# Performance work log

Hardware: AMD Instinct MI355X
Metric: run time of the kernel (lower is better)

Reference implementation:

```python
import jax, jax.numpy as jnp
import numpy as np
from jax import lax

F32 = jnp.float32
N_BATCH = 131072

# spiking gate algebra on {0,1} floats (matches VecAND/VecOR/VecXOR/VecNOT/VecMUX)
def OR(a, b):
    return a + b - a * b

def XOR(a, b):
    return a + b - 2.0 * a * b

def or_all(x):
    # OR-tree over last axis: 1 - prod(1-x)
    return 1.0 - jnp.prod(1.0 - x, axis=-1)

def and_all(x):
    return jnp.prod(x, axis=-1)

def const_bits(v, bits):
    # LSB-first constant bit vector
    return jnp.array([float((v >> i) & 1) for i in range(bits)], dtype=F32)

def ripple_add(A, B, cin):
    # VecRippleCarryAdder: A,B [N,bits] LSB-first, cin [N]
    P = XOR(A, B)
    G = A * B
    def step(c, pg):
        p, g = pg
        return OR(g, p * c), c
    cout, carries = lax.scan(step, cin, (jnp.moveaxis(P, -1, 0), jnp.moveaxis(G, -1, 0)))
    S = XOR(P, jnp.moveaxis(carries, 0, -1))
    return S, cout

def mul54(MA, MB):
    # VecArrayMultiplier54x54 (sequential accumulator): MA,MB [N,54] LSB-first -> [N,108]
    n = MA.shape[0]
    acc0 = jnp.zeros((n, 108), F32)
    Aext0 = jnp.concatenate([MA, jnp.zeros((n, 54), F32)], -1)
    zc = jnp.zeros((n,), F32)
    def step(carry, b):
        acc, Aext = carry
        acc, _ = ripple_add(acc, Aext * b[:, None], zc)  # add shifted partial product
        Aext = jnp.concatenate([jnp.zeros((n, 1), F32), Aext[:, :-1]], -1)  # <<1 (LSB-first)
        return (acc, Aext), None
    (acc, _), _ = lax.scan(step, (acc0, Aext0), jnp.moveaxis(MB, -1, 0))
    return acc

def lzd108(Xmsb):
    # VecLeadingZeroDetector108: X [N,108] MSB-first -> LZC [N,7] MSB-first
    n = Xmsb.shape[0]
    pos = jnp.asarray(np.array([[(i >> (6 - j)) & 1 for j in range(7)] for i in range(108)], dtype=np.float32))
    def step(state, inp):
        found, lzc = state
        bit, p = inp
        is_first = bit * (1.0 - found)
        lzc = is_first[:, None] * p[None, :] + (1.0 - is_first[:, None]) * lzc
        return (OR(found, is_first), lzc), None
    (found, lzc), _ = lax.scan(step, (jnp.zeros((n,), F32), jnp.zeros((n, 7), F32)),
                               (jnp.moveaxis(Xmsb, -1, 0), pos))
    az = (1.0 - found)[:, None]
    lzc = az * jnp.array([1, 1, 0, 1, 1, 0, 0], F32)[None, :] + (1.0 - az) * lzc  # all-zero -> 108
    return lzc

def barrel_left108(X, shift7):
    # VecBarrelShifterLeft108: X [N,108] MSB-first, shift7 [N,7] MSB-first
    cur = X
    for layer in range(7):
        amt = 2 ** (6 - layer)
        s = shift7[:, layer:layer + 1]
        if amt >= 108:
            shifted = jnp.zeros_like(cur)
        else:
            shifted = jnp.concatenate([cur[:, amt:], jnp.zeros_like(cur[:, :amt])], -1)
        cur = s * shifted + (1.0 - s) * cur
    return cur

def fp64_mul(A, B):
    n = A.shape[0]
    sA, eA, mA = A[:, 0], A[:, 1:12], A[:, 12:64]
    sB, eB, mB = B[:, 0], B[:, 1:12], B[:, 12:64]
    sign = XOR(sA, sB)
    eA_nz, eB_nz = or_all(eA), or_all(eB)
    # 54-bit LSB-first significands: [frac LSB..MSB, hidden, 0]
    MA = jnp.concatenate([mA[:, ::-1], eA_nz[:, None], jnp.zeros((n, 1), F32)], -1)
    MB = jnp.concatenate([mB[:, ::-1], eB_nz[:, None], jnp.zeros((n, 1), F32)], -1)
    P108 = mul54(MA, MB)  # LSB-first 108-bit product
    Xmsb = P108[:, ::-1]
    lzc = lzd108(Xmsb)
    norm = barrel_left108(Xmsb, lzc)
    mant53 = norm[:, :53]
    guard = norm[:, 53]
    sticky = or_all(norm[:, 54:108])  # 54-bit sticky OR-tree
    rnd = guard * OR(sticky, mant53[:, 52])  # round-to-nearest-even
    sum53, rcarry = ripple_add(mant53[:, ::-1], jnp.zeros((n, 53), F32), rnd)
    frac52 = sum53[:, :52][:, ::-1]  # MSB-first fraction (carry case yields all zeros)
    # 13-bit two's-complement exponent: eA + eB + 3 - 1023 - lzc + rcarry
    z2 = jnp.zeros((n, 2), F32)
    e13a = jnp.concatenate([eA[:, ::-1], z2], -1)
    e13b = jnp.concatenate([eB[:, ::-1], z2], -1)
    ones = jnp.ones((n,), F32)
    zer = jnp.zeros((n,), F32)
    E, _ = ripple_add(e13a, e13b, zer)
    E, _ = ripple_add(E, jnp.broadcast_to(const_bits(3, 13), (n, 13)), zer)
    E, _ = ripple_add(E, 1.0 - jnp.broadcast_to(const_bits(1023, 13), (n, 13)), ones)
    lzc13 = jnp.concatenate([lzc[:, ::-1], jnp.zeros((n, 6), F32)], -1)
    E, _ = ripple_add(E, 1.0 - lzc13, ones)
    E, _ = ripple_add(E, jnp.zeros((n, 13), F32), rcarry)
    neg = E[:, 12]
    e_zero = 1.0 - or_all(E)
    underflow = OR(neg, e_zero)  # E <= 0 -> flush to zero
    overflow = (1.0 - neg) * OR(E[:, 11], and_all(E[:, 0:11]))  # E >= 2047 -> inf
    exp11 = E[:, 0:11][:, ::-1]
    # special operands
    mA_nz, mB_nz = or_all(mA), or_all(mB)
    eA_ones, eB_ones = and_all(eA), and_all(eB)
    A_nan = eA_ones * mA_nz
    B_nan = eB_ones * mB_nz
    A_inf = eA_ones * (1.0 - mA_nz)
    B_inf = eB_ones * (1.0 - mB_nz)
    A_zero = (1.0 - eA_nz) * (1.0 - mA_nz)
    B_zero = (1.0 - eB_nz) * (1.0 - mB_nz)
    nan_sel = OR(OR(A_nan, B_nan), OR(A_inf * B_zero, B_inf * A_zero))
    inf_sel = OR(OR(A_inf, B_inf), overflow)
    zero_sel = OR(OR(A_zero, B_zero), underflow)
    def mux_vec(s, cvec, x):
        return s[:, None] * cvec[None, :] + (1.0 - s[:, None]) * x
    exp_o = mux_vec(zero_sel, jnp.zeros(11, F32), exp11)
    frac_o = mux_vec(zero_sel, jnp.zeros(52, F32), frac52)
    exp_o = mux_vec(inf_sel, jnp.ones(11, F32), exp_o)
    frac_o = mux_vec(inf_sel, jnp.zeros(52, F32), frac_o)
    qnan = jnp.zeros(52, F32).at[0].set(1.0)
    exp_o = mux_vec(nan_sel, jnp.ones(11, F32), exp_o)
    frac_o = mux_vec(nan_sel, qnan, frac_o)
    return jnp.concatenate([sign[:, None], exp_o, frac_o], -1)

def setup_inputs():
    key = jax.random.key(0)
    kA, kB = jax.random.split(key)
    A = jax.random.randint(kA, (N_BATCH, 64), 0, 2).astype(F32)
    B = jax.random.randint(kB, (N_BATCH, 64), 0, 2).astype(F32)
    return {"A": A, "B": B}

def reference(A, B):
    return fp64_mul(A, B)
```

## Files before the change

### kernel.cpp

```cpp
#include <hip/hip_runtime.h>

typedef unsigned long long u64;

__device__ __forceinline__ u64 fp64mul_circuit(u64 a, u64 b) {
    const u64 FRACM = 0xFFFFFFFFFFFFFULL;
    u64 sA = a >> 63, sB = b >> 63;
    unsigned eA = (unsigned)((a >> 52) & 0x7FF);
    unsigned eB = (unsigned)((b >> 52) & 0x7FF);
    u64 mA = a & FRACM, mB = b & FRACM;
    u64 sign = sA ^ sB;

    u64 MA = mA | ((u64)(eA != 0) << 52);
    u64 MB = mB | ((u64)(eB != 0) << 52);
    __uint128_t P = (__uint128_t)MA * (__uint128_t)MB;

    u64 hi = (u64)(P >> 64), lo = (u64)P;
    int lzc;
    if (hi)      lzc = __clzll(hi) - 20;
    else if (lo) lzc = 44 + __clzll(lo);
    else         lzc = 108;

    __uint128_t norm = P << lzc;

    u64 mant53     = (u64)(norm >> 55);
    unsigned guard = (unsigned)(((u64)(norm >> 54)) & 1);
    unsigned lsb   = (unsigned)(mant53 & 1);
    unsigned sticky = ((norm & ((((__uint128_t)1) << 54) - 1)) != 0) ? 1u : 0u;
    unsigned rnd   = guard & (sticky | lsb);

    u64 sum = mant53 + (u64)rnd;
    unsigned rcarry = (unsigned)((sum >> 53) & 1);
    u64 frac52 = sum & FRACM;

    int Emod = ((int)eA + (int)eB + 3 - 1023 - lzc + (int)rcarry) & 8191;
    int neg    = (Emod >> 12) & 1;
    int e_zero = (Emod == 0) ? 1 : 0;
    int underflow = neg | e_zero;
    int overflow  = (neg ^ 1) & ((((Emod >> 11) & 1) | ((Emod & 0x7FF) == 0x7FF)) ? 1 : 0);
    u64 exp11 = (u64)(Emod & 0x7FF);

    bool a_ones = (eA == 0x7FF), b_ones = (eB == 0x7FF);
    bool a_mnz = (mA != 0), b_mnz = (mB != 0);
    bool A_nan = a_ones && a_mnz,  B_nan = b_ones && b_mnz;
    bool A_inf = a_ones && !a_mnz, B_inf = b_ones && !b_mnz;
    bool A_zero = (eA == 0) && !a_mnz, B_zero = (eB == 0) && !b_mnz;

    bool nan_sel  = A_nan || B_nan || (A_inf && B_zero) || (B_inf && A_zero);
    bool inf_sel  = A_inf || B_inf || (overflow != 0);
    bool zero_sel = A_zero || B_zero || (underflow != 0);

    u64 expo = exp11, fraco = frac52;
    if (zero_sel) { expo = 0;     fraco = 0; }
    if (inf_sel)  { expo = 0x7FF; fraco = 0; }
    if (nan_sel)  { expo = 0x7FF; fraco = 1ULL << 51; }

    return (sign << 63) | (expo << 52) | fraco;
}

#define ROWS 16

__global__ __launch_bounds__(256) void spike_fp64_mul_kernel(
    const float* __restrict__ A, const float* __restrict__ B,
    float* __restrict__ out, int n)
{
    int gtid = blockIdx.x * blockDim.x + threadIdx.x;
    int wave = gtid >> 6;
    int lane = threadIdx.x & 63;
    int nwaves = n / ROWS;
    if (wave >= nwaves) return;

    size_t rowbase = (size_t)wave * ROWS;
    const float* pa = A + rowbase * 64 + lane;
    const float* pb = B + rowbase * 64 + lane;

    float va[ROWS], vb[ROWS];
    #pragma unroll
    for (int r = 0; r < ROWS; ++r) {
        va[r] = pa[(size_t)r * 64];
        vb[r] = pb[(size_t)r * 64];
    }

    u64 a = 0, b = 0;
    #pragma unroll
    for (int r = 0; r < ROWS; ++r) {
        u64 balA = __ballot(va[r] > 0.5f);
        u64 balB = __ballot(vb[r] > 0.5f);
        if (lane == r) { a = balA; b = balB; }
    }

    u64 res = fp64mul_circuit(__brevll(a), __brevll(b));

    float* po = out + rowbase * 64 + lane;
    #pragma unroll
    for (int r = 0; r < ROWS; ++r) {
        u64 v = __shfl(res, r);
        po[(size_t)r * 64] = (float)((v >> (63 - lane)) & 1);
    }
}

extern "C" void kernel_launch(void* const* d_in, const int* in_sizes, int n_in,
                              void* d_out, int out_size, void* d_ws, size_t ws_size,
                              hipStream_t stream) {
    const float* A = (const float*)d_in[0];
    const float* B = (const float*)d_in[1];
    float* out = (float*)d_out;
    int n = in_sizes[0] / 64;
    int nwaves = n / ROWS;
    int block = 256;
    int grid = (nwaves * 64 + block - 1) / block;
    spike_fp64_mul_kernel<<<grid, block, 0, stream>>>(A, B, out, n);
}
```

Baseline: 20.26 us.

## Use float4 loads/stores and LDS nibble packing instead of per-row ballots

```diff
diff --git a/kernel.cpp b/kernel.cpp
--- a/kernel.cpp
+++ b/kernel.cpp
@@ -58,43 +58,82 @@
 }
 
 #define ROWS 16
+#define WPB  4
 
 __global__ __launch_bounds__(256) void spike_fp64_mul_kernel(
     const float* __restrict__ A, const float* __restrict__ B,
     float* __restrict__ out, int n)
 {
-    int gtid = blockIdx.x * blockDim.x + threadIdx.x;
-    int wave = gtid >> 6;
+    __shared__ alignas(16) unsigned char nibA[WPB][ROWS][16];
+    __shared__ alignas(16) unsigned char nibB[WPB][ROWS][16];
+    __shared__ u64 resLds[WPB][ROWS];
+
     int lane = threadIdx.x & 63;
-    int nwaves = n / ROWS;
-    if (wave >= nwaves) return;
+    int wib  = threadIdx.x >> 6;
+    int wave = (blockIdx.x * blockDim.x + threadIdx.x) >> 6;
+    int k = lane >> 4;
+    int m = lane & 15;
 
     size_t rowbase = (size_t)wave * ROWS;
-    const float* pa = A + rowbase * 64 + lane;
-    const float* pb = B + rowbase * 64 + lane;
+    const float4* A4 = reinterpret_cast<const float4*>(A);
+    const float4* B4 = reinterpret_cast<const float4*>(B);
 
-    float va[ROWS], vb[ROWS];
+    float4 ra[4], rb[4];
     #pragma unroll
-    for (int r = 0; r < ROWS; ++r) {
-        va[r] = pa[(size_t)r * 64];
-        vb[r] = pb[(size_t)r * 64];
+    for (int j = 0; j < 4; ++j) {
+        int row = 4 * j + k;
+        ra[j] = A4[(rowbase + row) * 16 + m];
+        rb[j] = B4[(rowbase + row) * 16 + m];
+    }
+    #pragma unroll
+    for (int j = 0; j < 4; ++j) {
+        int row = 4 * j + k;
+        unsigned na = (unsigned)(ra[j].x > 0.5f)       | ((unsigned)(ra[j].y > 0.5f) << 1)
+                    | ((unsigned)(ra[j].z > 0.5f) << 2) | ((unsigned)(ra[j].w > 0.5f) << 3);
+        unsigned nb = (unsigned)(rb[j].x > 0.5f)       | ((unsigned)(rb[j].y > 0.5f) << 1)
+                    | ((unsigned)(rb[j].z > 0.5f) << 2) | ((unsigned)(rb[j].w > 0.5f) << 3);
+        nibA[wib][row][m] = (unsigned char)na;
+        nibB[wib][row][m] = (unsigned char)nb;
+    }
+    __syncthreads();
+
+    int rr = m;
+    uint4 wa = *reinterpret_cast<const uint4*>(nibA[wib][rr]);
+    uint4 wb = *reinterpret_cast<const uint4*>(nibB[wib][rr]);
+    u64 rowA = 0, rowB = 0;
+    {
+        unsigned va_[4] = {wa.x, wa.y, wa.z, wa.w};
+        unsigned vb_[4] = {wb.x, wb.y, wb.z, wb.w};
+        #pragma unroll
+        for (int q = 0; q < 4; ++q) {
+            unsigned v = va_[q] & 0x0F0F0F0Fu;
+            v = (v | (v >> 4)) & 0x00FF00FFu;
+            v = (v | (v >> 8)) & 0x0000FFFFu;
+            rowA |= (u64)v << (16 * q);
+            unsigned w = vb_[q] & 0x0F0F0F0Fu;
+            w = (w | (w >> 4)) & 0x00FF00FFu;
+            w = (w | (w >> 8)) & 0x0000FFFFu;
+            rowB |= (u64)w << (16 * q);
+        }
     }
 
-    u64 a = 0, b = 0;
+    u64 res = fp64mul_circuit(__brevll(rowA), __brevll(rowB));
+
+    if (lane < ROWS) resLds[wib][lane] = res;
+    __syncthreads();
+
+    float4* O4 = reinterpret_cast<float4*>(out);
     #pragma unroll
-    for (int r = 0; r < ROWS; ++r) {
-        u64 balA = __ballot(va[r] > 0.5f);
-        u64 balB = __ballot(vb[r] > 0.5f);
-        if (lane == r) { a = balA; b = balB; }
-    }
-
-    u64 res = fp64mul_circuit(__brevll(a), __brevll(b));
-
-    float* po = out + rowbase * 64 + lane;
-    #pragma unroll
-    for (int r = 0; r < ROWS; ++r) {
-        u64 v = __shfl(res, r);
-        po[(size_t)r * 64] = (float)((v >> (63 - lane)) & 1);
+    for (int i = 0; i < 4; ++i) {
+        int row = 4 * i + k;
+        u64 v = resLds[wib][row];
+        unsigned nib = (unsigned)(v >> (60 - 4 * m)) & 0xFu;
+        float4 o;
+        o.x = (float)((nib >> 3) & 1);
+        o.y = (float)((nib >> 2) & 1);
+        o.z = (float)((nib >> 1) & 1);
+        o.w = (float)(nib & 1);
+        O4[(rowbase + row) * 16 + m] = o;
     }
 }
 
@@ -105,8 +144,7 @@
     const float* B = (const float*)d_in[1];
     float* out = (float*)d_out;
     int n = in_sizes[0] / 64;
-    int nwaves = n / ROWS;
     int block = 256;
-    int grid = (nwaves * 64 + block - 1) / block;
+    int grid = n / 64;
     spike_fp64_mul_kernel<<<grid, block, 0, stream>>>(A, B, out, n);
 }
```

After: 19.92 us. About the same (-1.7%).
